# Optimization experiments

Measured on AMD Instinct MI355X. Metric: run time of the kernel, lower is better.

## Reference

```python
import jax, jax.numpy as jnp
import numpy as np

EMBED = 1024
MLP = 2048
N_EXPERTS = 8
TOP_K = 2


def setup_inputs() -> dict:
    key = jax.random.key(0)
    ks = jax.random.split(key, 5)
    scale_e = 1.0 / np.sqrt(EMBED)
    scale_m = 1.0 / np.sqrt(MLP)
    x = jax.random.normal(ks[0], (4, 2048, EMBED), dtype=jnp.float32)
    gate_w = jax.random.normal(ks[1], (EMBED, N_EXPERTS), dtype=jnp.float32) * scale_e
    w1 = jax.random.normal(ks[2], (N_EXPERTS, EMBED, MLP), dtype=jnp.float32) * scale_e
    w3 = jax.random.normal(ks[3], (N_EXPERTS, EMBED, MLP), dtype=jnp.float32) * scale_e
    w2 = jax.random.normal(ks[4], (N_EXPERTS, MLP, EMBED), dtype=jnp.float32) * scale_m
    return {"x": x, "gate_w": gate_w, "w1": w1, "w2": w2, "w3": w3}


def reference(x, gate_w, w1, w2, w3):
    B, S, D = x.shape
    xf = x.reshape(-1, D)  # [T, D] tokens
    # Router: softmax over experts, top-k select, renormalize selected weights
    router_logits = xf @ gate_w                      # [T, E]
    routing_weights = jax.nn.softmax(router_logits, axis=-1)
    sel_w, sel_e = jax.lax.top_k(routing_weights, TOP_K)  # [T, K]
    sel_w = sel_w / jnp.sum(sel_w, axis=-1, keepdims=True)
    out = jnp.zeros_like(xf)
    # Loop over the small fixed expert set; tokens not routed to expert e get
    # coefficient 0, matching the gather/scatter-add combine of the original.
    for e in range(N_EXPERTS):
        coef = jnp.sum(jnp.where(sel_e == e, sel_w, 0.0), axis=-1)  # [T]
        h = jax.nn.silu(xf @ w1[e]) * (xf @ w3[e])                  # [T, Mlp] SwiGLU
        out = out + coef[:, None] * (h @ w2[e])                     # [T, D]
    return out.reshape(B, S, D)
```

## Files before the change

### kernel.cpp

```cpp
#include <hip/hip_runtime.h>

#define EMBED 1024
#define MLP   2048
#define NE    8
#define NTOK  8192
#define RMAX  (2*NTOK + NE*256)

typedef _Float16 f16x8 __attribute__((ext_vector_type(8)));
typedef _Float16 f16x4 __attribute__((ext_vector_type(4)));
typedef float    f32x4 __attribute__((ext_vector_type(4)));

__device__ __forceinline__ void async_copy16(const void* g, void* l) {
  __builtin_amdgcn_global_load_lds(
      (const __attribute__((address_space(1))) unsigned int*)g,
      (__attribute__((address_space(3))) unsigned int*)l, 16, 0, 0);
}

__global__ __launch_bounds__(256) void router_kernel(
    const float* __restrict__ x, const float* __restrict__ gw,
    int* __restrict__ sel_e, float* __restrict__ sel_w, int* __restrict__ counts)
{
  __shared__ float gwt[NE * EMBED];
  __shared__ int cnt[NE];
  int tid = threadIdx.x;
  for (int idx = tid; idx < NE * EMBED; idx += 256) {
    int i = idx >> 3, e = idx & 7;
    gwt[e * EMBED + i] = gw[idx];
  }
  if (tid < NE) cnt[tid] = 0;
  __syncthreads();

  int lane = tid & 63, wv = tid >> 6;
  int t = blockIdx.x * 4 + wv;
  const float4* xr = (const float4*)(x + (size_t)t * EMBED);
  const float4* gt4 = (const float4*)gwt;
  float acc[NE];
  #pragma unroll
  for (int e = 0; e < NE; ++e) acc[e] = 0.f;
  #pragma unroll
  for (int c = 0; c < 4; ++c) {
    float4 xv = xr[c * 64 + lane];
    #pragma unroll
    for (int e = 0; e < NE; ++e) {
      float4 gv = gt4[e * 256 + c * 64 + lane];
      acc[e] += xv.x * gv.x + xv.y * gv.y + xv.z * gv.z + xv.w * gv.w;
    }
  }
  #pragma unroll
  for (int off = 1; off < 64; off <<= 1) {
    #pragma unroll
    for (int e = 0; e < NE; ++e) acc[e] += __shfl_xor(acc[e], off);
  }
  if (lane == 0) {
    int e0 = 0; float l0 = acc[0];
    #pragma unroll
    for (int e = 1; e < NE; ++e) if (acc[e] > l0) { l0 = acc[e]; e0 = e; }
    int e1 = -1; float l1 = -1e30f;
    #pragma unroll
    for (int e = 0; e < NE; ++e) if (e != e0 && acc[e] > l1) { l1 = acc[e]; e1 = e; }
    float w0 = 1.f / (1.f + expf(l1 - l0));
    sel_e[2 * t] = e0;     sel_w[2 * t] = w0;
    sel_e[2 * t + 1] = e1; sel_w[2 * t + 1] = 1.f - w0;
    atomicAdd(&cnt[e0], 1); atomicAdd(&cnt[e1], 1);
  }
  __syncthreads();
  if (tid < NE && cnt[tid]) atomicAdd(&counts[tid], cnt[tid]);
}

__global__ __launch_bounds__(256) void assign_kernel(
    const int* __restrict__ sel_e, const float* __restrict__ sel_w,
    const int* __restrict__ counts, int* __restrict__ cursor,
    int* __restrict__ offs_out, int* __restrict__ rowtok,
    float* __restrict__ rowcoef, int* __restrict__ inv)
{
  int offl[NE];
  {
    int o = 0;
    #pragma unroll
    for (int e = 0; e < NE; ++e) { offl[e] = o; o += (counts[e] + 255) & ~255; }
    if (blockIdx.x == 0 && threadIdx.x == 0) {
      #pragma unroll
      for (int e = 0; e < NE; ++e) offs_out[e] = offl[e];
      offs_out[NE] = o;
    }
  }
  int t = blockIdx.x * 256 + threadIdx.x;
  int lane = threadIdx.x & 63;
  #pragma unroll
  for (int k = 0; k < 2; ++k) {
    int e = sel_e[2 * t + k];
    float w = sel_w[2 * t + k];
    for (int xch = 0; xch < NE; ++xch) {
      unsigned long long m = __ballot(e == xch);
      if (e == xch) {
        int leader = __ffsll((unsigned long long)m) - 1;
        int base = 0;
        if (lane == leader) base = atomicAdd(&cursor[xch], (int)__popcll(m));
        base = __shfl(base, leader);
        int pos = offl[xch] + base + (int)__popcll(m & ((1ull << lane) - 1));
        rowtok[pos] = t;
        rowcoef[pos] = w;
        inv[2 * t + k] = pos;
      }
    }
  }
}

__global__ __launch_bounds__(256) void gather_kernel(
    const float* __restrict__ x, const int* __restrict__ rowtok,
    _Float16* __restrict__ xg)
{
  int r = blockIdx.x;
  int tok = rowtok[r];
  int t4 = threadIdx.x * 4;
  _Float16* dst = xg + (size_t)r * EMBED + t4;
  if (tok >= 0) {
    float4 v = *(const float4*)(x + (size_t)tok * EMBED + t4);
    f16x4 h; h.x = (_Float16)v.x; h.y = (_Float16)v.y; h.z = (_Float16)v.z; h.w = (_Float16)v.w;
    *(f16x4*)dst = h;
  } else {
    f16x4 z = {(_Float16)0.f, (_Float16)0.f, (_Float16)0.f, (_Float16)0.f};
    *(f16x4*)dst = z;
  }
}

__global__ __launch_bounds__(256) void transpose_all_kernel(
    const float* __restrict__ w1, const float* __restrict__ w3,
    const float* __restrict__ w2, _Float16* __restrict__ w1t,
    _Float16* __restrict__ w3t, _Float16* __restrict__ w2t)
{
  int id = blockIdx.x;
  int mat = id >> 12;
  int rr = id & 4095;
  int e = rr >> 9, tile = rr & 511;
  const float* src; _Float16* dst; int K, N;
  if (mat == 0)      { src = w1; dst = w1t; K = EMBED; N = MLP; }
  else if (mat == 1) { src = w3; dst = w3t; K = EMBED; N = MLP; }
  else               { src = w2; dst = w2t; K = MLP;   N = EMBED; }
  int nx = K >> 6;
  int k0 = (tile % nx) * 64, n0 = (tile / nx) * 64;
  src += (size_t)e * K * N;
  dst += (size_t)e * K * N;

  __shared__ float tilebuf[64][65];
  int t = threadIdx.x;
  int r = t >> 4, c4 = (t & 15) * 4;
  #pragma unroll
  for (int i = 0; i < 4; ++i) {
    float4 v = *(const float4*)(src + (size_t)(k0 + r + 16 * i) * N + n0 + c4);
    tilebuf[r + 16 * i][c4 + 0] = v.x;
    tilebuf[r + 16 * i][c4 + 1] = v.y;
    tilebuf[r + 16 * i][c4 + 2] = v.z;
    tilebuf[r + 16 * i][c4 + 3] = v.w;
  }
  __syncthreads();
  int kk8 = (t & 7) * 8, nIdx = t >> 3;
  #pragma unroll
  for (int i = 0; i < 2; ++i) {
    int n = nIdx + 32 * i;
    f16x8 h;
    #pragma unroll
    for (int j = 0; j < 8; ++j) h[j] = (_Float16)tilebuf[kk8 + j][n];
    *(f16x8*)(dst + (size_t)(n0 + n) * K + k0 + kk8) = h;
  }
}

__device__ __forceinline__ int resolve_expert(const int* __restrict__ offs, int r0)
{
  int e = 0;
  #pragma unroll
  for (int q = 0; q < NE - 1; ++q) if (r0 >= offs[q + 1]) e = q + 1;
  return e;
}

__device__ __forceinline__ const _Float16* frag_addr(const _Float16* buf, int row, int quad)
{
  return buf + row * 32 + ((quad ^ ((row >> 1) & 3)) << 3);
}

__global__ __launch_bounds__(512, 2) void gemm1_kernel(
    const _Float16* __restrict__ xg, const _Float16* __restrict__ w1t,
    const _Float16* __restrict__ w3t, const float* __restrict__ rowcoef,
    const int* __restrict__ offs, _Float16* __restrict__ hb)
{
  int r0 = blockIdx.x * 256;
  if (r0 >= offs[NE]) return;
  int e = resolve_expert(offs, r0);
  int n0 = blockIdx.y * 128;
  const _Float16* B1 = w1t + (size_t)e * MLP * EMBED;
  const _Float16* B3 = w3t + (size_t)e * MLP * EMBED;

  __shared__ __align__(16) _Float16 As[3][256 * 32];
  __shared__ __align__(16) _Float16 Bs1[3][128 * 32];
  __shared__ __align__(16) _Float16 Bs3[3][128 * 32];

  int tid = threadIdx.x, lane = tid & 63, wv = tid >> 6;
  int wm = (wv & 3) << 6, wn = (wv >> 2) << 6;
  int l16 = lane & 15, quad = lane >> 4;

  int rowA0 = tid >> 2, kqpA = tid & 3;
  int rowA1 = rowA0 + 128;
  int kqlA0 = kqpA ^ ((rowA0 >> 1) & 3);
  int kqlA1 = kqpA ^ ((rowA1 >> 1) & 3);
  int rowB = tid >> 2, kqpB = tid & 3;
  int kqlB = kqpB ^ ((rowB >> 1) & 3);
  size_t gA0 = (size_t)(r0 + rowA0) * EMBED + kqlA0 * 8;
  size_t gA1 = (size_t)(r0 + rowA1) * EMBED + kqlA1 * 8;
  size_t gB  = (size_t)(n0 + rowB) * EMBED + kqlB * 8;
  int lofA0 = (wv * 64) * 8;
  int lofA1 = (512 + wv * 64) * 8;
  int lofB  = (wv * 64) * 8;

  f32x4 acc1[4][4], acc3[4][4];
  f32x4 z4 = {0.f, 0.f, 0.f, 0.f};
  #pragma unroll
  for (int i = 0; i < 4; ++i)
    #pragma unroll
    for (int j = 0; j < 4; ++j) { acc1[i][j] = z4; acc3[i][j] = z4; }

  auto stage = [&](int b, int kk) {
    async_copy16(xg + gA0 + kk, &As[b][lofA0]);
    async_copy16(xg + gA1 + kk, &As[b][lofA1]);
    async_copy16(B1 + gB  + kk, &Bs1[b][lofB]);
    async_copy16(B3 + gB  + kk, &Bs3[b][lofB]);
  };

  const int NIT = EMBED / 32;
  stage(0, 0);
  for (int k = 0; k < NIT; ++k) {
    int b = k % 3;
    if (k + 1 < NIT) {
      stage((k + 1) % 3, (k + 1) * 32);
      asm volatile("s_waitcnt vmcnt(4)" ::: "memory");
    } else {
      asm volatile("s_waitcnt vmcnt(0)" ::: "memory");
    }
    asm volatile("s_barrier" ::: "memory");

    f16x8 af[4], b1f[4], b3f[4];
    #pragma unroll
    for (int i = 0; i < 4; ++i)
      af[i] = *(const f16x8*)frag_addr(As[b], wm + 16 * i + l16, quad);
    #pragma unroll
    for (int j = 0; j < 4; ++j) {
      b1f[j] = *(const f16x8*)frag_addr(Bs1[b], wn + 16 * j + l16, quad);
      b3f[j] = *(const f16x8*)frag_addr(Bs3[b], wn + 16 * j + l16, quad);
    }
    #pragma unroll
    for (int i = 0; i < 4; ++i)
      #pragma unroll
      for (int j = 0; j < 4; ++j) {
        acc1[i][j] = __builtin_amdgcn_mfma_f32_16x16x32_f16(af[i], b1f[j], acc1[i][j], 0, 0, 0);
        acc3[i][j] = __builtin_amdgcn_mfma_f32_16x16x32_f16(af[i], b3f[j], acc3[i][j], 0, 0, 0);
      }
  }

  #pragma unroll
  for (int i = 0; i < 4; ++i) {
    int mb = r0 + wm + 16 * i + quad * 4;
    float cf[4];
    #pragma unroll
    for (int rg = 0; rg < 4; ++rg) cf[rg] = rowcoef[mb + rg];
    #pragma unroll
    for (int j = 0; j < 4; ++j) {
      int col = n0 + wn + 16 * j + l16;
      #pragma unroll
      for (int rg = 0; rg < 4; ++rg) {
        float g = acc1[i][j][rg], u = acc3[i][j][rg];
        float h = g * u * cf[rg] / (1.f + __expf(-g));
        hb[(size_t)(mb + rg) * MLP + col] = (_Float16)h;
      }
    }
  }
}

__global__ __launch_bounds__(512, 2) void gemm2_kernel(
    const _Float16* __restrict__ hb, const _Float16* __restrict__ w2t,
    const int* __restrict__ offs, _Float16* __restrict__ hb2)
{
  int r0 = blockIdx.x * 256;
  if (r0 >= offs[NE]) return;
  int e = resolve_expert(offs, r0);
  int n0 = blockIdx.y * 128;
  const _Float16* B = w2t + (size_t)e * EMBED * MLP;

  __shared__ __align__(16) _Float16 As[3][256 * 32];
  __shared__ __align__(16) _Float16 Bs[3][128 * 32];

  int tid = threadIdx.x, lane = tid & 63, wv = tid >> 6;
  int wm = (wv & 3) << 6, wn = (wv >> 2) << 6;
  int l16 = lane & 15, quad = lane >> 4;

  int rowA0 = tid >> 2, kqpA = tid & 3;
  int rowA1 = rowA0 + 128;
  int kqlA0 = kqpA ^ ((rowA0 >> 1) & 3);
  int kqlA1 = kqpA ^ ((rowA1 >> 1) & 3);
  int rowB = tid >> 2, kqpB = tid & 3;
  int kqlB = kqpB ^ ((rowB >> 1) & 3);
  size_t gA0 = (size_t)(r0 + rowA0) * MLP + kqlA0 * 8;
  size_t gA1 = (size_t)(r0 + rowA1) * MLP + kqlA1 * 8;
  size_t gB  = (size_t)(n0 + rowB) * MLP + kqlB * 8;
  int lofA0 = (wv * 64) * 8;
  int lofA1 = (512 + wv * 64) * 8;
  int lofB  = (wv * 64) * 8;

  f32x4 acc[4][4];
  f32x4 z4 = {0.f, 0.f, 0.f, 0.f};
  #pragma unroll
  for (int i = 0; i < 4; ++i)
    #pragma unroll
    for (int j = 0; j < 4; ++j) acc[i][j] = z4;

  auto stage = [&](int b, int kk) {
    async_copy16(hb + gA0 + kk, &As[b][lofA0]);
    async_copy16(hb + gA1 + kk, &As[b][lofA1]);
    async_copy16(B  + gB  + kk, &Bs[b][lofB]);
  };

  const int NIT = MLP / 32;
  stage(0, 0);
  for (int k = 0; k < NIT; ++k) {
    int b = k % 3;
    if (k + 1 < NIT) {
      stage((k + 1) % 3, (k + 1) * 32);
      asm volatile("s_waitcnt vmcnt(3)" ::: "memory");
    } else {
      asm volatile("s_waitcnt vmcnt(0)" ::: "memory");
    }
    asm volatile("s_barrier" ::: "memory");

    f16x8 af[4], bf[4];
    #pragma unroll
    for (int i = 0; i < 4; ++i)
      af[i] = *(const f16x8*)frag_addr(As[b], wm + 16 * i + l16, quad);
    #pragma unroll
    for (int j = 0; j < 4; ++j)
      bf[j] = *(const f16x8*)frag_addr(Bs[b], wn + 16 * j + l16, quad);
    #pragma unroll
    for (int i = 0; i < 4; ++i)
      #pragma unroll
      for (int j = 0; j < 4; ++j)
        acc[i][j] = __builtin_amdgcn_mfma_f32_16x16x32_f16(af[i], bf[j], acc[i][j], 0, 0, 0);
  }

  #pragma unroll
  for (int i = 0; i < 4; ++i) {
    int mb = r0 + wm + 16 * i + quad * 4;
    #pragma unroll
    for (int j = 0; j < 4; ++j) {
      int col = n0 + wn + 16 * j + l16;
      #pragma unroll
      for (int rg = 0; rg < 4; ++rg)
        hb2[(size_t)(mb + rg) * EMBED + col] = (_Float16)acc[i][j][rg];
    }
  }
}

__global__ __launch_bounds__(256) void combine_kernel(
    const _Float16* __restrict__ hb2, const int* __restrict__ inv,
    float* __restrict__ out)
{
  int t = blockIdx.x;
  int d = threadIdx.x * 4;
  int p0 = inv[2 * t], p1 = inv[2 * t + 1];
  f16x4 a = *(const f16x4*)(hb2 + (size_t)p0 * EMBED + d);
  f16x4 b = *(const f16x4*)(hb2 + (size_t)p1 * EMBED + d);
  float4 r;
  r.x = (float)a.x + (float)b.x;
  r.y = (float)a.y + (float)b.y;
  r.z = (float)a.z + (float)b.z;
  r.w = (float)a.w + (float)b.w;
  *(float4*)(out + (size_t)t * EMBED + d) = r;
}

extern "C" void kernel_launch(void* const* d_in, const int* in_sizes, int n_in,
                              void* d_out, int out_size, void* d_ws, size_t ws_size,
                              hipStream_t stream)
{
  (void)in_sizes; (void)n_in; (void)ws_size; (void)out_size;
  const float* x  = (const float*)d_in[0];
  const float* gw = (const float*)d_in[1];
  const float* w1 = (const float*)d_in[2];
  const float* w2 = (const float*)d_in[3];
  const float* w3 = (const float*)d_in[4];
  float* out = (float*)d_out;
  char* ws = (char*)d_ws;

  size_t o = 0;
  auto alloc = [&](size_t bytes) { size_t r = o; o = (o + bytes + 255) & ~255ULL; return r; };
  const size_t wbytes = (size_t)NE * MLP * EMBED * 2;
  _Float16* w1t = (_Float16*)(ws + alloc(wbytes));
  _Float16* w3t = (_Float16*)(ws + alloc(wbytes));
  _Float16* w2t = (_Float16*)(ws + alloc(wbytes));
  _Float16* xg  = (_Float16*)(ws + alloc((size_t)RMAX * EMBED * 2));
  _Float16* hb  = (_Float16*)(ws + alloc((size_t)RMAX * MLP * 2));
  int*   rowtok  = (int*)(ws + alloc((size_t)RMAX * 4));
  float* rowcoef = (float*)(ws + alloc((size_t)RMAX * 4));
  int*   sel_e   = (int*)(ws + alloc((size_t)2 * NTOK * 4));
  float* sel_w   = (float*)(ws + alloc((size_t)2 * NTOK * 4));
  int*   inv     = (int*)(ws + alloc((size_t)2 * NTOK * 4));
  int*   meta    = (int*)(ws + alloc(256));
  int* counts = meta;
  int* offs   = meta + 8;
  int* cursor = meta + 17;
  _Float16* hb2 = xg;

  hipMemsetAsync(meta, 0, 256, stream);
  hipMemsetAsync(rowtok, 0xFF, (size_t)RMAX * 4, stream);
  hipMemsetAsync(rowcoef, 0, (size_t)RMAX * 4, stream);

  transpose_all_kernel<<<3 * 4096, 256, 0, stream>>>(w1, w3, w2, w1t, w3t, w2t);

  router_kernel<<<NTOK / 4, 256, 0, stream>>>(x, gw, sel_e, sel_w, counts);
  assign_kernel<<<NTOK / 256, 256, 0, stream>>>(sel_e, sel_w, counts, cursor,
                                                offs, rowtok, rowcoef, inv);
  gather_kernel<<<RMAX, 256, 0, stream>>>(x, rowtok, xg);

  gemm1_kernel<<<dim3(RMAX / 256, MLP / 128), 512, 0, stream>>>(xg, w1t, w3t, rowcoef, offs, hb);
  gemm2_kernel<<<dim3(RMAX / 256, EMBED / 128), 512, 0, stream>>>(hb, w2t, offs, hb2);
  combine_kernel<<<NTOK, 256, 0, stream>>>(hb2, inv, out);
}
```

Measured before the change: 626.2 us.

## Switch GEMMs to double-buffered pipeline and shrink gemm2 tile to 128x128

```diff
diff --git a/kernel.cpp b/kernel.cpp
--- a/kernel.cpp
+++ b/kernel.cpp
@@ -190,9 +190,9 @@
   const _Float16* B1 = w1t + (size_t)e * MLP * EMBED;
   const _Float16* B3 = w3t + (size_t)e * MLP * EMBED;
 
-  __shared__ __align__(16) _Float16 As[3][256 * 32];
-  __shared__ __align__(16) _Float16 Bs1[3][128 * 32];
-  __shared__ __align__(16) _Float16 Bs3[3][128 * 32];
+  __shared__ __align__(16) _Float16 As[2][256 * 32];
+  __shared__ __align__(16) _Float16 Bs1[2][128 * 32];
+  __shared__ __align__(16) _Float16 Bs3[2][128 * 32];
 
   int tid = threadIdx.x, lane = tid & 63, wv = tid >> 6;
   int wm = (wv & 3) << 6, wn = (wv >> 2) << 6;
@@ -228,14 +228,10 @@
   const int NIT = EMBED / 32;
   stage(0, 0);
   for (int k = 0; k < NIT; ++k) {
-    int b = k % 3;
-    if (k + 1 < NIT) {
-      stage((k + 1) % 3, (k + 1) * 32);
-      asm volatile("s_waitcnt vmcnt(4)" ::: "memory");
-    } else {
-      asm volatile("s_waitcnt vmcnt(0)" ::: "memory");
-    }
+    int b = k & 1;
+    asm volatile("s_waitcnt vmcnt(0)" ::: "memory");
     asm volatile("s_barrier" ::: "memory");
+    if (k + 1 < NIT) stage((k + 1) & 1, (k + 1) * 32);
 
     f16x8 af[4], b1f[4], b3f[4];
     #pragma unroll
@@ -274,35 +270,33 @@
   }
 }
 
-__global__ __launch_bounds__(512, 2) void gemm2_kernel(
+__global__ __launch_bounds__(256, 3) void gemm2_kernel(
     const _Float16* __restrict__ hb, const _Float16* __restrict__ w2t,
     const int* __restrict__ offs, _Float16* __restrict__ hb2)
 {
-  int r0 = blockIdx.x * 256;
+  int r0 = blockIdx.x * 128;
   if (r0 >= offs[NE]) return;
   int e = resolve_expert(offs, r0);
   int n0 = blockIdx.y * 128;
   const _Float16* B = w2t + (size_t)e * EMBED * MLP;
 
-  __shared__ __align__(16) _Float16 As[3][256 * 32];
-  __shared__ __align__(16) _Float16 Bs[3][128 * 32];
+  __shared__ __align__(16) _Float16 As[2][128 * 32];
+  __shared__ __align__(16) _Float16 Bs[2][128 * 32];
 
   int tid = threadIdx.x, lane = tid & 63, wv = tid >> 6;
-  int wm = (wv & 3) << 6, wn = (wv >> 2) << 6;
+  int wm = (wv & 1) << 6, wn = (wv >> 1) << 6;
   int l16 = lane & 15, quad = lane >> 4;
 
-  int rowA0 = tid >> 2, kqpA = tid & 3;
-  int rowA1 = rowA0 + 128;
-  int kqlA0 = kqpA ^ ((rowA0 >> 1) & 3);
-  int kqlA1 = kqpA ^ ((rowA1 >> 1) & 3);
-  int rowB = tid >> 2, kqpB = tid & 3;
-  int kqlB = kqpB ^ ((rowB >> 1) & 3);
-  size_t gA0 = (size_t)(r0 + rowA0) * MLP + kqlA0 * 8;
-  size_t gA1 = (size_t)(r0 + rowA1) * MLP + kqlA1 * 8;
-  size_t gB  = (size_t)(n0 + rowB) * MLP + kqlB * 8;
-  int lofA0 = (wv * 64) * 8;
-  int lofA1 = (512 + wv * 64) * 8;
-  int lofB  = (wv * 64) * 8;
+  int row0 = tid >> 2,         kqp = tid & 3;
+  int row1 = (256 + tid) >> 2;
+  int kql0 = kqp ^ ((row0 >> 1) & 3);
+  int kql1 = kqp ^ ((row1 >> 1) & 3);
+  size_t gA0 = (size_t)(r0 + row0) * MLP + kql0 * 8;
+  size_t gA1 = (size_t)(r0 + row1) * MLP + kql1 * 8;
+  size_t gB0 = (size_t)(n0 + row0) * MLP + kql0 * 8;
+  size_t gB1 = (size_t)(n0 + row1) * MLP + kql1 * 8;
+  int lof0 = (wv * 64) * 8;
+  int lof1 = (256 + wv * 64) * 8;
 
   f32x4 acc[4][4];
   f32x4 z4 = {0.f, 0.f, 0.f, 0.f};
@@ -312,22 +306,19 @@
     for (int j = 0; j < 4; ++j) acc[i][j] = z4;
 
   auto stage = [&](int b, int kk) {
-    async_copy16(hb + gA0 + kk, &As[b][lofA0]);
-    async_copy16(hb + gA1 + kk, &As[b][lofA1]);
-    async_copy16(B  + gB  + kk, &Bs[b][lofB]);
+    async_copy16(hb + gA0 + kk, &As[b][lof0]);
+    async_copy16(hb + gA1 + kk, &As[b][lof1]);
+    async_copy16(B  + gB0 + kk, &Bs[b][lof0]);
+    async_copy16(B  + gB1 + kk, &Bs[b][lof1]);
   };
 
   const int NIT = MLP / 32;
   stage(0, 0);
   for (int k = 0; k < NIT; ++k) {
-    int b = k % 3;
-    if (k + 1 < NIT) {
-      stage((k + 1) % 3, (k + 1) * 32);
-      asm volatile("s_waitcnt vmcnt(3)" ::: "memory");
-    } else {
-      asm volatile("s_waitcnt vmcnt(0)" ::: "memory");
-    }
+    int b = k & 1;
+    asm volatile("s_waitcnt vmcnt(0)" ::: "memory");
     asm volatile("s_barrier" ::: "memory");
+    if (k + 1 < NIT) stage((k + 1) & 1, (k + 1) * 32);
 
     f16x8 af[4], bf[4];
     #pragma unroll
@@ -417,6 +408,6 @@
   gather_kernel<<<RMAX, 256, 0, stream>>>(x, rowtok, xg);
 
   gemm1_kernel<<<dim3(RMAX / 256, MLP / 128), 512, 0, stream>>>(xg, w1t, w3t, rowcoef, offs, hb);
-  gemm2_kernel<<<dim3(RMAX / 256, EMBED / 128), 512, 0, stream>>>(hb, w2t, offs, hb2);
+  gemm2_kernel<<<dim3(RMAX / 128, EMBED / 128), 256, 0, stream>>>(hb, w2t, offs, hb2);
   combine_kernel<<<NTOK, 256, 0, stream>>>(hb2, inv, out);
 }
```

Result: slower. 688.4 us (+9.9%).
